# Kernel tuning notes

Measured on AMD Instinct MI355X. Metric: run time of the kernel, lower is better.

## Reference

```python
import jax, jax.numpy as jnp
import numpy as np

T, B, V, HID, L = 1024, 64, 256, 512, 2


def setup_inputs() -> dict:
    key = jax.random.key(0)
    ks = jax.random.split(key, 6)
    inputs = jax.random.normal(ks[0], (T, B, V), jnp.float32)
    H = jax.random.normal(ks[1], (L, B, HID), jnp.float32) * 0.1
    s1 = 1.0 / np.sqrt(V + HID)   # torch Linear default init bound
    W_net = jax.random.uniform(ks[2], (HID, V + HID), jnp.float32, -s1, s1)
    b_net = jax.random.uniform(ks[3], (HID,), jnp.float32, -s1, s1)
    s2 = 1.0 / np.sqrt(2 * HID)
    W_deep = jax.random.uniform(ks[4], (HID, 2 * HID), jnp.float32, -s2, s2)
    b_deep = jax.random.uniform(ks[5], (HID,), jnp.float32, -s2, s2)
    return {"inputs": inputs, "H": H, "W_net": W_net, "b_net": b_net,
            "W_deep": W_deep, "b_deep": b_deep}


def _rnn_scan(xs, h0, W, b):
    # xs: [T, B, Din], h0: [B, HID]; torch does tanh(cat(x, h) @ W.T + b)
    Din = xs.shape[-1]
    Wx, Wh = W[:, :Din], W[:, Din:]  # split cat-matmul into two GEMMs (same math)
    def step(h, x):
        h = jnp.tanh(x @ Wx.T + h @ Wh.T + b)
        return h, h
    last, states = jax.lax.scan(step, h0, xs)
    return states, last  # [T, B, HID], [B, HID]


def reference(inputs, H, W_net, b_net, W_deep, b_deep):
    all_states, last = _rnn_scan(inputs, H[0], W_net, b_net)
    last_states = [last]
    for l in range(1, H.shape[0]):  # deep layers: input dim = HID
        all_states, last = _rnn_scan(all_states, H[l], W_deep, b_deep)
        last_states.append(last)
    return all_states, jnp.stack(last_states)  # [T,B,HID], [L,B,HID]
```

## Files before the change

kernel.cpp:

```cpp
#include <hip/hip_runtime.h>
#include <hip/hip_fp16.h>
#include <cstdint>
#include <cstddef>

#define TT 1024
#define BB 64
#define VV 256
#define HH 512
static const size_t TBH = (size_t)TT * BB * HH;

#define AGENT __HIP_MEMORY_SCOPE_AGENT

typedef _Float16 half2v __attribute__((ext_vector_type(2)));
union U32H2 { unsigned u; half2v h; };

__device__ __forceinline__ unsigned pack_f16x2(float a, float b) {
    __half ha = __float2half_rn(a);
    __half hb = __float2half_rn(b);
    return (unsigned)__half_as_ushort(ha) | ((unsigned)__half_as_ushort(hb) << 16);
}

__device__ __forceinline__ float tanh_fast(float x) {
    float ax = fabsf(x);
    float e = __expf(-2.0f * ax);
    float r = (1.0f - e) * __builtin_amdgcn_rcpf(1.0f + e);
    return copysignf(r, x);
}

__device__ __forceinline__ float fdot2(unsigned w, unsigned h, float acc) {
    U32H2 uw; uw.u = w;
    U32H2 uh; uh.u = h;
#if __has_builtin(__builtin_amdgcn_fdot2)
    return __builtin_amdgcn_fdot2(uw.h, uh.h, acc, false);
#else
    return acc + (float)uw.h[0] * (float)uh.h[0] + (float)uw.h[1] * (float)uh.h[1];
#endif
}

__global__ void pack_weights(const float* __restrict__ Wnet,
                             const float* __restrict__ Wdeep,
                             unsigned* __restrict__ Wq0, unsigned* __restrict__ Wq1,
                             unsigned* __restrict__ Wp0, unsigned* __restrict__ Wp1) {
    int id = blockIdx.x * 256 + threadIdx.x;
    const int NQ  = HH * (HH / 2);
    const int NP0 = (VV / 2) * HH;
    const int NP1 = (HH / 2) * HH;
    if (id < NQ) {
        int i = id >> 8, jp = id & 255;
        const float* row = Wnet + (size_t)i * (VV + HH) + VV;
        Wq0[id] = pack_f16x2(row[2 * jp], row[2 * jp + 1]);
        return;
    }
    id -= NQ;
    if (id < NQ) {
        int i = id >> 8, jp = id & 255;
        const float* row = Wdeep + (size_t)i * (2 * HH) + HH;
        Wq1[id] = pack_f16x2(row[2 * jp], row[2 * jp + 1]);
        return;
    }
    id -= NQ;
    if (id < NP0) {
        int k2 = id >> 9, n = id & 511;
        const float* row = Wnet + (size_t)n * (VV + HH);
        Wp0[id] = pack_f16x2(row[2 * k2], row[2 * k2 + 1]);
        return;
    }
    id -= NP0;
    if (id < NP1) {
        int k2 = id >> 9, n = id & 511;
        const float* row = Wdeep + (size_t)n * (2 * HH);
        Wp1[id] = pack_f16x2(row[2 * k2], row[2 * k2 + 1]);
        return;
    }
}

__device__ __forceinline__ void dot8(float* acc, unsigned a, uint4 w0, uint4 w1) {
    acc[0] = fdot2(w0.x, a, acc[0]);
    acc[1] = fdot2(w0.y, a, acc[1]);
    acc[2] = fdot2(w0.z, a, acc[2]);
    acc[3] = fdot2(w0.w, a, acc[3]);
    acc[4] = fdot2(w1.x, a, acc[4]);
    acc[5] = fdot2(w1.y, a, acc[5]);
    acc[6] = fdot2(w1.z, a, acc[6]);
    acc[7] = fdot2(w1.w, a, acc[7]);
}

__launch_bounds__(1024)
__global__ void xproj_f16(const float* __restrict__ A,
                          const unsigned* __restrict__ Wp,
                          const float* __restrict__ bias,
                          float* __restrict__ C, int K) {
    extern __shared__ unsigned As2[];
    const int m0 = blockIdx.x * 32;
    const int t = threadIdx.x;
    const int K2 = K >> 1;

    const int nf4 = 8 * K;
    const float4* Ag = (const float4*)(A + (size_t)m0 * K);
    for (int idx = t; idx < nf4; idx += 1024) {
        float4 v = Ag[idx];
        As2[idx * 2]     = pack_f16x2(v.x, v.y);
        As2[idx * 2 + 1] = pack_f16x2(v.z, v.w);
    }
    __syncthreads();

    const int rg = t >> 6;
    const int n0 = (t & 63) * 8;

    float acc0[8] = {0, 0, 0, 0, 0, 0, 0, 0};
    float acc1[8] = {0, 0, 0, 0, 0, 0, 0, 0};

    const unsigned* a0p = As2 + (size_t)(rg * 2) * K2;
    const unsigned* a1p = a0p + K2;

#pragma unroll 4
    for (int k2 = 0; k2 < K2; k2 += 2) {
        unsigned a00 = a0p[k2], a01 = a0p[k2 + 1];
        unsigned a10 = a1p[k2], a11 = a1p[k2 + 1];
        const uint4 w00 = *(const uint4*)(Wp + (size_t)k2 * 512 + n0);
        const uint4 w01 = *(const uint4*)(Wp + (size_t)k2 * 512 + n0 + 4);
        const uint4 w10 = *(const uint4*)(Wp + (size_t)(k2 + 1) * 512 + n0);
        const uint4 w11 = *(const uint4*)(Wp + (size_t)(k2 + 1) * 512 + n0 + 4);
        dot8(acc0, a00, w00, w01);
        dot8(acc1, a10, w00, w01);
        dot8(acc0, a01, w10, w11);
        dot8(acc1, a11, w10, w11);
    }

    float bv[8];
#pragma unroll
    for (int c = 0; c < 8; ++c) bv[c] = bias[n0 + c];

    float* Crow0 = C + (size_t)(m0 + rg * 2) * 512 + n0;
    float* Crow1 = Crow0 + 512;
    *(float4*)(Crow0)     = make_float4(acc0[0] + bv[0], acc0[1] + bv[1], acc0[2] + bv[2], acc0[3] + bv[3]);
    *(float4*)(Crow0 + 4) = make_float4(acc0[4] + bv[4], acc0[5] + bv[5], acc0[6] + bv[6], acc0[7] + bv[7]);
    *(float4*)(Crow1)     = make_float4(acc1[0] + bv[0], acc1[1] + bv[1], acc1[2] + bv[2], acc1[3] + bv[3]);
    *(float4*)(Crow1 + 4) = make_float4(acc1[4] + bv[4], acc1[5] + bv[5], acc1[6] + bv[6], acc1[7] + bv[7]);
}

__launch_bounds__(512, 1)
__global__ void rnn_scan3(const unsigned* __restrict__ Wq,
                          const float* __restrict__ h0,
                          float* __restrict__ states,
                          float* __restrict__ last,
                          unsigned long long* __restrict__ X) {
    __shared__ unsigned short hsh16[2][256];

    const int w = blockIdx.x;
    const int b = w & 63;
    const int s = w >> 6;
    const int r = threadIdx.x;
    const int lane = r & 63;
    const int owner = r >> 8;
    const bool is_owner = (owner == s);

    uint4 wreg[32];
    {
        const uint4* Wr = (const uint4*)(Wq + (size_t)r * 256 + s * 128);
#pragma unroll
        for (int q = 0; q < 32; ++q) wreg[q] = Wr[q];
    }
#pragma unroll
    for (int q = 0; q < 32; ++q)
        asm volatile("" : "+v"(wreg[q].x), "+v"(wreg[q].y),
                          "+v"(wreg[q].z), "+v"(wreg[q].w));

    unsigned hp[2];
    {
        const float2* h2 = (const float2*)(h0 + (size_t)b * HH);
#pragma unroll
        for (int rr = 0; rr < 2; ++rr) {
            float2 v = h2[s * 128 + rr * 64 + lane];
            hp[rr] = pack_f16x2(v.x, v.y);
        }
    }

    unsigned long long* slotA = X + ((((size_t)b * 2 + owner) * 2 + 0) << 8) + (r & 255);
    unsigned long long* slotB = slotA + 256;

    size_t base = (size_t)b * HH;
    const size_t tstride = (size_t)BB * HH;

    float pre_cur = 0.f;
    if (is_owner) pre_cur = states[base + r];

    float h = 0.f;
    for (int t = 0; t < TT; ++t) {
        float pre_nxt = 0.f;
        if (is_owner && t + 1 < TT) pre_nxt = states[base + tstride + r];

        float a0 = 0.f, a1 = 0.f, a2 = 0.f, a3 = 0.f;
#pragma unroll
        for (int q = 0; q < 32; ++q) {
            const uint4 wv = wreg[q];
            const int j = q * 4;
            unsigned s0 = (unsigned)__builtin_amdgcn_readlane((int)hp[(j + 0) >> 6], (j + 0) & 63);
            unsigned s1 = (unsigned)__builtin_amdgcn_readlane((int)hp[(j + 1) >> 6], (j + 1) & 63);
            unsigned s2 = (unsigned)__builtin_amdgcn_readlane((int)hp[(j + 2) >> 6], (j + 2) & 63);
            unsigned s3 = (unsigned)__builtin_amdgcn_readlane((int)hp[(j + 3) >> 6], (j + 3) & 63);
            a0 = fdot2(wv.x, s0, a0);
            a1 = fdot2(wv.y, s1, a1);
            a2 = fdot2(wv.z, s2, a2);
            a3 = fdot2(wv.w, s3, a3);
        }
        float part = (a0 + a1) + (a2 + a3);

        const int p = t & 1;
        unsigned long long* slot = p ? slotB : slotA;
        if (!is_owner) {
            unsigned long long msg = ((unsigned long long)(unsigned)(t + 1) << 32)
                                   | (unsigned long long)__float_as_uint(part);
            __hip_atomic_store(slot, msg, __ATOMIC_RELAXED, AGENT);
        } else {
            unsigned long long v;
            do {
                v = __hip_atomic_load(slot, __ATOMIC_RELAXED, AGENT);
            } while ((unsigned)(v >> 32) != (unsigned)(t + 1));
            float pother = __uint_as_float((unsigned)v);
            h = tanh_fast(pre_cur + part + pother);
            states[base + r] = h;
            hsh16[p][r & 255] = __half_as_ushort(__float2half_rn(h));
        }
        __syncthreads();

        const unsigned* hh = (const unsigned*)hsh16[p];
#pragma unroll
        for (int rr = 0; rr < 2; ++rr) hp[rr] = hh[rr * 64 + lane];

        pre_cur = pre_nxt;
        base += tstride;
    }

    if (is_owner) last[(size_t)b * HH + r] = h;
}

extern "C" void kernel_launch(void* const* d_in, const int* in_sizes, int n_in,
                              void* d_out, int out_size, void* d_ws, size_t ws_size,
                              hipStream_t stream) {
    (void)in_sizes; (void)n_in; (void)out_size; (void)ws_size;
    const float* inputs = (const float*)d_in[0];
    const float* H      = (const float*)d_in[1];
    const float* Wnet   = (const float*)d_in[2];
    const float* bnet   = (const float*)d_in[3];
    const float* Wdeep  = (const float*)d_in[4];
    const float* bdeep  = (const float*)d_in[5];
    float* out = (float*)d_out;

    unsigned long long* X = (unsigned long long*)d_ws;
    unsigned* Wq0 = (unsigned*)(X + 64 * 2 * 2 * 256);
    unsigned* Wq1 = Wq0 + HH * (HH / 2);
    unsigned* Wp0 = Wq1 + HH * (HH / 2);
    unsigned* Wp1 = Wp0 + (VV / 2) * HH;

    hipLaunchKernelGGL(pack_weights, dim3(1792), dim3(256), 0, stream,
                       Wnet, Wdeep, Wq0, Wq1, Wp0, Wp1);

    hipLaunchKernelGGL(xproj_f16, dim3((TT * BB) / 32), dim3(1024),
                       32 * (VV / 2) * sizeof(unsigned), stream,
                       inputs, Wp0, bnet, out, VV);

    hipLaunchKernelGGL(rnn_scan3, dim3(128), dim3(512), 0, stream,
                       Wq0, H, out, out + TBH, X);

    hipLaunchKernelGGL(xproj_f16, dim3((TT * BB) / 32), dim3(1024),
                       32 * (HH / 2) * sizeof(unsigned), stream,
                       out, Wp1, bdeep, out, HH);

    hipLaunchKernelGGL(rnn_scan3, dim3(128), dim3(512), 0, stream,
                       Wq1, H + (size_t)BB * HH, out, out + TBH + (size_t)BB * HH, X);
}
```

Before: 4.037 ms.

## Split recurrent matvec by output rows across blocks, exchanging hidden states

Replaces the K-split scan, where each block held half the K dimension for all 512 rows and exchanged partial sums, with a row split: each block owns 256 output rows over the full K, reduced by cross-lane shuffles. Blocks now exchange finished h values through global slots, and the full h vector is rebuilt in swizzled LDS and read as uint4 vectors instead of via readlane broadcasts. This is meant to cut the per-step readlane scalar overhead and to let both blocks apply tanh in parallel. In exchange it adds shuffle reductions and leaves only half the lanes doing finalize work while the rest poll.

```diff
diff --git a/kernel.cpp b/kernel.cpp
--- a/kernel.cpp
+++ b/kernel.cpp
@@ -35,6 +35,12 @@
 #else
     return acc + (float)uw.h[0] * (float)uh.h[0] + (float)uw.h[1] * (float)uh.h[1];
 #endif
+}
+
+__device__ __forceinline__ int swz_us(int r) {
+    int j = r >> 1;
+    int js = j ^ (((j >> 5) & 7) << 2);
+    return (js << 1) | (r & 1);
 }
 
 __global__ void pack_weights(const float* __restrict__ Wnet,
@@ -140,99 +146,117 @@
 }
 
 __launch_bounds__(512, 1)
-__global__ void rnn_scan3(const unsigned* __restrict__ Wq,
+__global__ void rnn_scan4(const unsigned* __restrict__ Wq,
                           const float* __restrict__ h0,
                           float* __restrict__ states,
                           float* __restrict__ last,
                           unsigned long long* __restrict__ X) {
-    __shared__ unsigned short hsh16[2][256];
-
-    const int w = blockIdx.x;
-    const int b = w & 63;
-    const int s = w >> 6;
-    const int r = threadIdx.x;
-    const int lane = r & 63;
-    const int owner = r >> 8;
-    const bool is_owner = (owner == s);
-
-    uint4 wreg[32];
+    __shared__ unsigned short hsh[2][512];
+
+    const int wg = blockIdx.x;
+    const int b = wg & 63;
+    const int s = wg >> 6;
+    const int tid = threadIdx.x;
+    const int w = tid >> 6;
+    const int lane = tid & 63;
+    const int rowsub = lane & 7;
+    const int kg = lane >> 3;
+    const int rbase = s * 256 + w * 32 + rowsub;
+    const bool is_fin = (kg < 4);
+    const int rfin = rbase + 8 * kg;
+    const int fidx = w * 32 + rowsub + 8 * kg;
+    const int pidx = w * 32 + (lane & 31);
+    const int rpoll = (1 - s) * 256 + pidx;
+
+    uint4 wreg[4][8];
+#pragma unroll
+    for (int j = 0; j < 4; ++j) {
+        const uint4* Wr = (const uint4*)(Wq + (size_t)(rbase + 8 * j) * 256 + kg * 32);
+#pragma unroll
+        for (int q = 0; q < 8; ++q) wreg[j][q] = Wr[q];
+    }
+
+    hsh[1][swz_us(tid)] = __half_as_ushort(__float2half_rn(h0[(size_t)b * HH + tid]));
+    __syncthreads();
+    uint4 hv[8];
     {
-        const uint4* Wr = (const uint4*)(Wq + (size_t)r * 256 + s * 128);
-#pragma unroll
-        for (int q = 0; q < 32; ++q) wreg[q] = Wr[q];
-    }
-#pragma unroll
-    for (int q = 0; q < 32; ++q)
-        asm volatile("" : "+v"(wreg[q].x), "+v"(wreg[q].y),
-                          "+v"(wreg[q].z), "+v"(wreg[q].w));
-
-    unsigned hp[2];
-    {
-        const float2* h2 = (const float2*)(h0 + (size_t)b * HH);
-#pragma unroll
-        for (int rr = 0; rr < 2; ++rr) {
-            float2 v = h2[s * 128 + rr * 64 + lane];
-            hp[rr] = pack_f16x2(v.x, v.y);
-        }
-    }
-
-    unsigned long long* slotA = X + ((((size_t)b * 2 + owner) * 2 + 0) << 8) + (r & 255);
-    unsigned long long* slotB = slotA + 256;
+        const uint4* hb = (const uint4*)hsh[1];
+#pragma unroll
+        for (int q = 0; q < 8; ++q) hv[q] = hb[kg * 8 + (q ^ kg)];
+    }
+
+    unsigned long long* slotW_A = X + (((size_t)(b * 2 + s) * 2 + 0) << 8) + fidx;
+    unsigned long long* slotW_B = slotW_A + 256;
+    unsigned long long* slotR_A = X + (((size_t)(b * 2 + (1 - s)) * 2 + 0) << 8) + pidx;
+    unsigned long long* slotR_B = slotR_A + 256;
 
     size_t base = (size_t)b * HH;
     const size_t tstride = (size_t)BB * HH;
 
     float pre_cur = 0.f;
-    if (is_owner) pre_cur = states[base + r];
-
-    float h = 0.f;
+    if (is_fin) pre_cur = states[base + rfin];
+
+    float hlast = 0.f;
     for (int t = 0; t < TT; ++t) {
         float pre_nxt = 0.f;
-        if (is_owner && t + 1 < TT) pre_nxt = states[base + tstride + r];
+        if (is_fin && t + 1 < TT) pre_nxt = states[base + tstride + rfin];
 
         float a0 = 0.f, a1 = 0.f, a2 = 0.f, a3 = 0.f;
 #pragma unroll
-        for (int q = 0; q < 32; ++q) {
-            const uint4 wv = wreg[q];
-            const int j = q * 4;
-            unsigned s0 = (unsigned)__builtin_amdgcn_readlane((int)hp[(j + 0) >> 6], (j + 0) & 63);
-            unsigned s1 = (unsigned)__builtin_amdgcn_readlane((int)hp[(j + 1) >> 6], (j + 1) & 63);
-            unsigned s2 = (unsigned)__builtin_amdgcn_readlane((int)hp[(j + 2) >> 6], (j + 2) & 63);
-            unsigned s3 = (unsigned)__builtin_amdgcn_readlane((int)hp[(j + 3) >> 6], (j + 3) & 63);
-            a0 = fdot2(wv.x, s0, a0);
-            a1 = fdot2(wv.y, s1, a1);
-            a2 = fdot2(wv.z, s2, a2);
-            a3 = fdot2(wv.w, s3, a3);
+        for (int q = 0; q < 8; ++q) {
+            const uint4 hq = hv[q];
+            a0 = fdot2(wreg[0][q].x, hq.x, a0);
+            a0 = fdot2(wreg[0][q].y, hq.y, a0);
+            a0 = fdot2(wreg[0][q].z, hq.z, a0);
+            a0 = fdot2(wreg[0][q].w, hq.w, a0);
+            a1 = fdot2(wreg[1][q].x, hq.x, a1);
+            a1 = fdot2(wreg[1][q].y, hq.y, a1);
+            a1 = fdot2(wreg[1][q].z, hq.z, a1);
+            a1 = fdot2(wreg[1][q].w, hq.w, a1);
+            a2 = fdot2(wreg[2][q].x, hq.x, a2);
+            a2 = fdot2(wreg[2][q].y, hq.y, a2);
+            a2 = fdot2(wreg[2][q].z, hq.z, a2);
+            a2 = fdot2(wreg[2][q].w, hq.w, a2);
+            a3 = fdot2(wreg[3][q].x, hq.x, a3);
+            a3 = fdot2(wreg[3][q].y, hq.y, a3);
+            a3 = fdot2(wreg[3][q].z, hq.z, a3);
+            a3 = fdot2(wreg[3][q].w, hq.w, a3);
         }
-        float part = (a0 + a1) + (a2 + a3);
+        a0 += __shfl_xor(a0, 8);  a0 += __shfl_xor(a0, 16);  a0 += __shfl_xor(a0, 32);
+        a1 += __shfl_xor(a1, 8);  a1 += __shfl_xor(a1, 16);  a1 += __shfl_xor(a1, 32);
+        a2 += __shfl_xor(a2, 8);  a2 += __shfl_xor(a2, 16);  a2 += __shfl_xor(a2, 32);
+        a3 += __shfl_xor(a3, 8);  a3 += __shfl_xor(a3, 16);  a3 += __shfl_xor(a3, 32);
 
         const int p = t & 1;
-        unsigned long long* slot = p ? slotB : slotA;
-        if (!is_owner) {
+        if (is_fin) {
+            float af = (kg == 0) ? a0 : (kg == 1) ? a1 : (kg == 2) ? a2 : a3;
+            float h = tanh_fast(pre_cur + af);
+            hlast = h;
+            states[base + rfin] = h;
             unsigned long long msg = ((unsigned long long)(unsigned)(t + 1) << 32)
-                                   | (unsigned long long)__float_as_uint(part);
-            __hip_atomic_store(slot, msg, __ATOMIC_RELAXED, AGENT);
+                                   | (unsigned long long)__float_as_uint(h);
+            __hip_atomic_store(p ? slotW_B : slotW_A, msg, __ATOMIC_RELAXED, AGENT);
+            hsh[p][swz_us(rfin)] = __half_as_ushort(__float2half_rn(h));
         } else {
+            unsigned long long* slot = p ? slotR_B : slotR_A;
             unsigned long long v;
             do {
                 v = __hip_atomic_load(slot, __ATOMIC_RELAXED, AGENT);
             } while ((unsigned)(v >> 32) != (unsigned)(t + 1));
-            float pother = __uint_as_float((unsigned)v);
-            h = tanh_fast(pre_cur + part + pother);
-            states[base + r] = h;
-            hsh16[p][r & 255] = __half_as_ushort(__float2half_rn(h));
+            float hp_ = __uint_as_float((unsigned)v);
+            hsh[p][swz_us(rpoll)] = __half_as_ushort(__float2half_rn(hp_));
         }
         __syncthreads();
 
-        const unsigned* hh = (const unsigned*)hsh16[p];
-#pragma unroll
-        for (int rr = 0; rr < 2; ++rr) hp[rr] = hh[rr * 64 + lane];
+        const uint4* hb = (const uint4*)hsh[p];
+#pragma unroll
+        for (int q = 0; q < 8; ++q) hv[q] = hb[kg * 8 + (q ^ kg)];
 
         pre_cur = pre_nxt;
         base += tstride;
     }
 
-    if (is_owner) last[(size_t)b * HH + r] = h;
+    if (is_fin) last[(size_t)b * HH + rfin] = hlast;
 }
 
 extern "C" void kernel_launch(void* const* d_in, const int* in_sizes, int n_in,
@@ -260,13 +284,13 @@
                        32 * (VV / 2) * sizeof(unsigned), stream,
                        inputs, Wp0, bnet, out, VV);
 
-    hipLaunchKernelGGL(rnn_scan3, dim3(128), dim3(512), 0, stream,
+    hipLaunchKernelGGL(rnn_scan4, dim3(128), dim3(512), 0, stream,
                        Wq0, H, out, out + TBH, X);
 
     hipLaunchKernelGGL(xproj_f16, dim3((TT * BB) / 32), dim3(1024),
                        32 * (HH / 2) * sizeof(unsigned), stream,
                        out, Wp1, bdeep, out, HH);
 
-    hipLaunchKernelGGL(rnn_scan3, dim3(128), dim3(512), 0, stream,
+    hipLaunchKernelGGL(rnn_scan4, dim3(128), dim3(512), 0, stream,
                        Wq1, H + (size_t)BB * HH, out, out + TBH + (size_t)BB * HH, X);
 }
```

Result: slower. 4.253 ms (+5.4%).
